# Kernel tuning notes

Measured on AMD Instinct MI355X. Metric: run time of the kernel, lower is better.

## Reference

```python
import jax, jax.numpy as jnp
import numpy as np

D_MODEL = 512
NHEAD = 8
HEAD_DIM = D_MODEL // NHEAD  # 64
ROTARY_DIM = HEAD_DIM        # rotary_dim defaults to head_dim
WINDOW = (127, 128)          # (left, right) sliding window, flash-attn convention
ROPE_BASE = 10000.0


def setup_inputs() -> dict:
    key = jax.random.key(0)
    k1, k2, k3, k4 = jax.random.split(key, 4)
    N, T = 4, 2048
    x = jax.random.normal(k1, (N, T, D_MODEL), dtype=jnp.float32)
    # Wqkv: Linear(d_model, 3*d_model, bias=False) -> weight [3*D, D]
    Wqkv_w = jax.random.normal(k2, (3 * D_MODEL, D_MODEL), dtype=jnp.float32) * (D_MODEL ** -0.5)
    # out_proj: Linear(d_model, d_model, bias=True)
    out_w = jax.random.normal(k3, (D_MODEL, D_MODEL), dtype=jnp.float32) * (D_MODEL ** -0.5)
    out_b = jax.random.normal(k4, (D_MODEL,), dtype=jnp.float32) * 0.01
    return {"x": x, "Wqkv_w": Wqkv_w, "out_w": out_w, "out_b": out_b}


def _rope_cos_sin(T, dtype):
    # flash-attn RotaryEmbedding: inv_freq over even indices of rotary_dim
    inv_freq = 1.0 / (ROPE_BASE ** (jnp.arange(0, ROTARY_DIM, 2, dtype=jnp.float32) / ROTARY_DIM))
    t = jnp.arange(T, dtype=jnp.float32)
    freqs = jnp.outer(t, inv_freq)  # [T, ROTARY_DIM//2]
    return jnp.cos(freqs).astype(dtype), jnp.sin(freqs).astype(dtype)


def _apply_rotary(x, cos, sin):
    # non-interleaved (rotate halves); x: [N, T, H, hd], rotary over first ROTARY_DIM dims
    r, rest = x[..., :ROTARY_DIM], x[..., ROTARY_DIM:]
    half = ROTARY_DIM // 2
    x1, x2 = r[..., :half], r[..., half:]
    c = cos[None, :, None, :]  # [1, T, 1, half]
    s = sin[None, :, None, :]
    rotated = jnp.concatenate([x1 * c - x2 * s, x2 * c + x1 * s], axis=-1)
    return jnp.concatenate([rotated, rest], axis=-1) if rest.shape[-1] else rotated


def reference(x, Wqkv_w, out_w, out_b):
    N, T, D = x.shape
    qkv = jnp.einsum('ntd,ed->nte', x, Wqkv_w).reshape(N, T, 3, NHEAD, HEAD_DIM)
    q, k, v = qkv[:, :, 0], qkv[:, :, 1], qkv[:, :, 2]  # each [N, T, H, hd]
    cos, sin = _rope_cos_sin(T, x.dtype)
    q = _apply_rotary(q, cos, sin)
    k = _apply_rotary(k, cos, sin)
    scale = HEAD_DIM ** -0.5
    scores = jnp.einsum('nthd,nshd->nhts', q, k) * scale  # [N, H, T, T]
    # sliding window: query i attends key j iff i - left <= j <= i + right
    i = jnp.arange(T)[:, None]
    j = jnp.arange(T)[None, :]
    mask = (j >= i - WINDOW[0]) & (j <= i + WINDOW[1])  # [T, T]
    scores = jnp.where(mask[None, None], scores, jnp.finfo(scores.dtype).min)
    attn = jax.nn.softmax(scores, axis=-1)
    ctx = jnp.einsum('nhts,nshd->nthd', attn, v).reshape(N, T, D)
    return jnp.einsum('ntd,ed->nte', ctx, out_w) + out_b
```

## Files before the change

### kernel.cpp

```cpp
#include <hip/hip_runtime.h>
#include <math.h>

#define TSEQ 2048
#define NB 4
#define DM 512
#define NH 8
#define HD 64

typedef _Float16 half8 __attribute__((ext_vector_type(8)));
typedef _Float16 half4 __attribute__((ext_vector_type(4)));
typedef float floatx4 __attribute__((ext_vector_type(4)));

#if __has_builtin(__builtin_amdgcn_exp2f)
#define EXP2F(x) __builtin_amdgcn_exp2f(x)
#else
#define EXP2F(x) exp2f(x)
#endif

__device__ __forceinline__ void gl2lds16(const _Float16* g, _Float16* l) {
  const __attribute__((address_space(1))) unsigned int* gp =
      (const __attribute__((address_space(1))) unsigned int*)(uintptr_t)g;
  __attribute__((address_space(3))) unsigned int* lp =
      (__attribute__((address_space(3))) unsigned int*)(uintptr_t)l;
  __builtin_amdgcn_global_load_lds(gp, lp, 16, 0, 0);
}


__device__ __forceinline__ void cvt8(const float* __restrict__ src, char* __restrict__ dst,
                                     int unit_src, int unit_dst) {
  const float4 a = ((const float4*)src)[2 * unit_src];
  const float4 b = ((const float4*)src)[2 * unit_src + 1];
  half8 h;
  h[0] = (_Float16)a.x; h[1] = (_Float16)a.y; h[2] = (_Float16)a.z; h[3] = (_Float16)a.w;
  h[4] = (_Float16)b.x; h[5] = (_Float16)b.y; h[6] = (_Float16)b.z; h[7] = (_Float16)b.w;
  *(half8*)(dst + (size_t)unit_dst * 16) = h;
}

__global__ void prep(const float* __restrict__ x, const float* __restrict__ wqkv,
                     const float* __restrict__ ow, char* __restrict__ ws) {
  const int i = blockIdx.x * 256 + threadIdx.x;
  if (i < 524288) {
    cvt8(x, ws, i, i);
  } else if (i < 622592) {
    const int o = i - 524288;
    cvt8(wqkv, ws + 8650752, o, o);
  } else if (i < 655360) {
    const int o = i - 622592;
    cvt8(ow, ws + 10485760, o, o);
  } else {
    const int u = i - 655360;
    float4 o4;
    {
      const int id = 2 * u, t = id >> 5, fi = id & 31;
      const float invf = powf(10000.0f, -(float)(2 * fi) * (1.0f / 64.0f));
      float s, c; sincosf((float)t * invf, &s, &c);
      o4.x = c; o4.y = s;
    }
    {
      const int id = 2 * u + 1, t = id >> 5, fi = id & 31;
      const float invf = powf(10000.0f, -(float)(2 * fi) * (1.0f / 64.0f));
      float s, c; sincosf((float)t * invf, &s, &c);
      o4.z = c; o4.w = s;
    }
    ((float4*)(ws + 46137344))[u] = o4;
  }
}

__global__ __launch_bounds__(256) void qkv_gemm_mfma(
    const _Float16* __restrict__ A, const _Float16* __restrict__ B,
    const float2* __restrict__ rope,
    _Float16* __restrict__ qb, _Float16* __restrict__ kb, _Float16* __restrict__ vT)
{
  __shared__ __align__(16) _Float16 As[128 * 32];
  __shared__ __align__(16) _Float16 Bs[128 * 32];
  const int tid = threadIdx.x;
  const int wv = tid >> 6, lane = tid & 63, quad = lane >> 4, col = lane & 15;
  const int wm = wv >> 1, we = wv & 1;
  const int m0 = blockIdx.x << 7, c0 = blockIdx.y << 7;
  const int r0 = tid >> 2, p0 = tid & 3;
  const int cA0 = (p0 - (r0 >> 1)) & 3;
  const int r1 = (tid + 256) >> 2, p1 = tid & 3;
  const int cA1 = (p1 - (r1 >> 1)) & 3;
  const _Float16* ga0 = &A[(size_t)(m0 + r0) * DM + cA0 * 8];
  const _Float16* ga1 = &A[(size_t)(m0 + r1) * DM + cA1 * 8];
  const _Float16* gb0 = &B[(size_t)(c0 + r0) * DM + cA0 * 8];
  const _Float16* gb1 = &B[(size_t)(c0 + r1) * DM + cA1 * 8];
  _Float16* la0 = &As[tid * 8];
  _Float16* la1 = &As[(tid + 256) * 8];
  _Float16* lb0 = &Bs[tid * 8];
  _Float16* lb1 = &Bs[(tid + 256) * 8];
  floatx4 acc[4][4] = {};
  for (int k0 = 0; k0 < DM; k0 += 32) {
    __syncthreads();
    gl2lds16(ga0 + k0, la0);
    gl2lds16(ga1 + k0, la1);
    gl2lds16(gb0 + k0, lb0);
    gl2lds16(gb1 + k0, lb1);
    __syncthreads();
    half8 af[4], bf[4];
#pragma unroll
    for (int mt = 0; mt < 4; mt++) {
      const int R = wm * 64 + mt * 16 + col;
      af[mt] = *(const half8*)&As[R * 32 + (((quad + (R >> 1)) & 3) << 3)];
    }
#pragma unroll
    for (int et = 0; et < 4; et++) {
      const int R = we * 64 + et * 16 + col;
      bf[et] = *(const half8*)&Bs[R * 32 + (((quad + (R >> 1)) & 3) << 3)];
    }
#pragma unroll
    for (int mt = 0; mt < 4; mt++)
#pragma unroll
      for (int et = 0; et < 4; et++)
        acc[mt][et] = __builtin_amdgcn_mfma_f32_16x16x32_f16(af[mt], bf[et], acc[mt][et], 0, 0, 0);
  }
  const int eidx = (c0 >> 6) + we;
  const int three = eidx >> 3, h = eidx & 7;
  const int mbase = m0 + wm * 64 + quad * 4;
  if (three == 2) {
#pragma unroll
    for (int mt = 0; mt < 4; mt++) {
      const int m = mbase + mt * 16;
      const int n = m >> 11, t = m & 2047;
#pragma unroll
      for (int et = 0; et < 4; et++) {
        const int dh = et * 16 + col;
        half4 hv;
#pragma unroll
        for (int r = 0; r < 4; r++) hv[r] = (_Float16)acc[mt][et][r];
        *(half4*)&vT[(size_t)(n * NH + h) * HD * TSEQ + (size_t)dh * TSEQ + t] = hv;
      }
    }
  } else {
    _Float16* dst = three ? kb : qb;
    const float scl = three ? 1.0f : 0.125f * 1.4426950408889634f;
#pragma unroll
    for (int mt = 0; mt < 4; mt++)
#pragma unroll
      for (int r = 0; r < 4; r++) {
        const int m = mbase + mt * 16 + r;
        const int n = m >> 11, t = m & 2047;
#pragma unroll
        for (int et = 0; et < 4; et++) {
          const int i = ((et & 1) << 4) + col;
          const float2 cs = rope[t * 32 + i];
          const float v = acc[mt][et][r];
          const float v2 = acc[mt][et ^ 2][r];
          const float o = (et < 2) ? (v * cs.x - v2 * cs.y) : (v * cs.x + v2 * cs.y);
          dst[((size_t)(n * NH + h) * TSEQ + t) * HD + et * 16 + col] = (_Float16)(o * scl);
        }
      }
  }
}

__global__ __launch_bounds__(256, 4) void attn_win_mfma(
    const _Float16* __restrict__ qb, const _Float16* __restrict__ kb,
    const _Float16* __restrict__ vT, _Float16* __restrict__ ctx)
{
  __shared__ __align__(16) char smem[36864];
  _Float16* Ks = (_Float16*)smem;
  _Float16* Vt = (_Float16*)(smem + 9216);
  _Float16* Ps = (_Float16*)(smem + 18432);
  _Float16* Osh = (_Float16*)(smem + 27648);

  const int tid = threadIdx.x;
  const int wv = tid >> 6;
  const int lane = tid & 63;
  const int quad = lane >> 4;
  const int col = lane & 15;
  const int nh = blockIdx.y;
  const int q0 = blockIdx.x << 6;
  const _Float16* qp = qb + (size_t)nh * TSEQ * HD;
  const _Float16* kp = kb + (size_t)nh * TSEQ * HD;
  const _Float16* vp = vT + (size_t)nh * HD * TSEQ;

  const int i_row = (wv << 4) + col;
  const int ig = q0 + i_row;
  const half8 qf0 = *(const half8*)&qp[(size_t)ig * HD + (quad << 3)];
  const half8 qf1 = *(const half8*)&qp[(size_t)ig * HD + 32 + (quad << 3)];

  float l_i = 0.0f;
  floatx4 accO[4] = {};

  const int kt0 = max(0, q0 - 127) >> 6;
  const int kt1 = min(TSEQ - 1, q0 + 191) >> 6;
  const int kr = tid >> 2, kc = (tid & 3) << 4;
  const int vd = tid >> 2, vc = (tid & 3) << 4;
  const _Float16* kpr = kp + (size_t)kr * HD + kc;
  const _Float16* vpr = vp + (size_t)vd * TSEQ + vc;

  half8 ck0 = *(const half8*)(kpr + (size_t)(kt0 << 6) * HD);
  half8 ck1 = *(const half8*)(kpr + (size_t)(kt0 << 6) * HD + 8);
  half8 cv0 = *(const half8*)(vpr + (kt0 << 6));
  half8 cv1 = *(const half8*)(vpr + (kt0 << 6) + 8);

  for (int kt = kt0; kt <= kt1; kt++) {
    const int j0 = kt << 6;
    __syncthreads();
    *(half8*)&Ks[kr * 72 + kc] = ck0;
    *(half8*)&Ks[kr * 72 + kc + 8] = ck1;
    *(half8*)&Vt[vd * 72 + vc] = cv0;
    *(half8*)&Vt[vd * 72 + vc + 8] = cv1;
    __syncthreads();

    {
      const int jn = (kt < kt1) ? (j0 + 64) : j0;
      ck0 = *(const half8*)(kpr + (size_t)jn * HD);
      ck1 = *(const half8*)(kpr + (size_t)jn * HD + 8);
      cv0 = *(const half8*)(vpr + jn);
      cv1 = *(const half8*)(vpr + jn + 8);
    }

    floatx4 S[4];
#pragma unroll
    for (int js = 0; js < 4; js++) {
      const half8 a0 = *(const half8*)&Ks[((js << 4) + col) * 72 + (quad << 3)];
      const half8 a1 = *(const half8*)&Ks[((js << 4) + col) * 72 + 32 + (quad << 3)];
      floatx4 c = {0.f, 0.f, 0.f, 0.f};
      c = __builtin_amdgcn_mfma_f32_16x16x32_f16(a0, qf0, c, 0, 0, 0);
      c = __builtin_amdgcn_mfma_f32_16x16x32_f16(a1, qf1, c, 0, 0, 0);
      S[js] = c;
    }
    const int relb = j0 - ig + 127 + (quad << 2);
#pragma unroll
    for (int js = 0; js < 4; js++) {
      half4 ph;
#pragma unroll
      for (int r = 0; r < 4; r++) {
        const bool valid = (unsigned)(relb + (js << 4) + r) < 256u;
        const float p = valid ? EXP2F(S[js][r]) : 0.0f;
        l_i += p;
        ph[r] = (_Float16)p;
      }
      *(half4*)&Ps[i_row * 72 + (js << 4) + (quad << 2)] = ph;
    }
    const half8 pa0 = *(const half8*)&Ps[i_row * 72 + (quad << 3)];
    const half8 pa1 = *(const half8*)&Ps[i_row * 72 + 32 + (quad << 3)];
#pragma unroll
    for (int d4 = 0; d4 < 4; d4++) {
      const half8 vb0 = *(const half8*)&Vt[((d4 << 4) + col) * 72 + (quad << 3)];
      const half8 vb1 = *(const half8*)&Vt[((d4 << 4) + col) * 72 + 32 + (quad << 3)];
      accO[d4] = __builtin_amdgcn_mfma_f32_16x16x32_f16(pa0, vb0, accO[d4], 0, 0, 0);
      accO[d4] = __builtin_amdgcn_mfma_f32_16x16x32_f16(pa1, vb1, accO[d4], 0, 0, 0);
    }
  }
  l_i += __shfl_xor(l_i, 16, 64);
  l_i += __shfl_xor(l_i, 32, 64);
  {
    const float linv = 1.0f / l_i;
    float l4[4];
#pragma unroll
    for (int r = 0; r < 4; r++) l4[r] = __shfl(linv, (quad << 2) + r, 64);
#pragma unroll
    for (int d4 = 0; d4 < 4; d4++)
#pragma unroll
      for (int r = 0; r < 4; r++)
        Osh[((wv << 4) + (quad << 2) + r) * 72 + (d4 << 4) + col] = (_Float16)(accO[d4][r] * l4[r]);
  }
  __syncthreads();
  {
    const int n = nh >> 3, h = nh & 7;
    const int oi = tid >> 2, oc = (tid & 3) << 4;
    _Float16* dst = &ctx[((size_t)n * TSEQ + q0 + oi) * DM + h * HD + oc];
    *(half8*)&dst[0] = *(const half8*)&Osh[oi * 72 + oc];
    *(half8*)&dst[8] = *(const half8*)&Osh[oi * 72 + oc + 8];
  }
}

__global__ __launch_bounds__(256) void out_gemm_mfma(
    const _Float16* __restrict__ A, const _Float16* __restrict__ B,
    const float* __restrict__ bias, float* __restrict__ out)
{
  __shared__ _Float16 As[128 * 40];
  __shared__ _Float16 Bs[64 * 40];
  const int tid = threadIdx.x;
  const int wv = tid >> 6, lane = tid & 63, quad = lane >> 4, col = lane & 15;
  const int wm = wv >> 1, we = wv & 1;
  const int m0 = blockIdx.x << 7, c0 = blockIdx.y << 6;
  const int sr = tid >> 1, sc = (tid & 1) << 4;
  const int br = tid >> 2, bc = (tid & 3) << 3;
  const _Float16* ap = &A[(size_t)(m0 + sr) * DM + sc];
  const _Float16* bp = &B[(size_t)(c0 + br) * DM + bc];
  floatx4 acc[4][2] = {};
  for (int k0 = 0; k0 < DM; k0 += 32) {
    const half8 a0 = *(const half8*)(ap + k0);
    const half8 a1 = *(const half8*)(ap + k0 + 8);
    const half8 b0 = *(const half8*)(bp + k0);
    __syncthreads();
    *(half8*)&As[sr * 40 + sc] = a0;
    *(half8*)&As[sr * 40 + sc + 8] = a1;
    *(half8*)&Bs[br * 40 + bc] = b0;
    __syncthreads();
    half8 af[4], bf[2];
#pragma unroll
    for (int mt = 0; mt < 4; mt++)
      af[mt] = *(const half8*)&As[(wm * 64 + mt * 16 + col) * 40 + quad * 8];
#pragma unroll
    for (int et = 0; et < 2; et++)
      bf[et] = *(const half8*)&Bs[(we * 32 + et * 16 + col) * 40 + quad * 8];
#pragma unroll
    for (int mt = 0; mt < 4; mt++)
#pragma unroll
      for (int et = 0; et < 2; et++)
        acc[mt][et] = __builtin_amdgcn_mfma_f32_16x16x32_f16(af[mt], bf[et], acc[mt][et], 0, 0, 0);
  }
  float bb[2];
#pragma unroll
  for (int et = 0; et < 2; et++) bb[et] = bias[c0 + we * 32 + et * 16 + col];
  const int mbase = m0 + wm * 64 + quad * 4;
#pragma unroll
  for (int mt = 0; mt < 4; mt++)
#pragma unroll
    for (int r = 0; r < 4; r++) {
      const int m = mbase + mt * 16 + r;
#pragma unroll
      for (int et = 0; et < 2; et++)
        out[(size_t)m * DM + c0 + we * 32 + et * 16 + col] = acc[mt][et][r] + bb[et];
    }
}

extern "C" void kernel_launch(void* const* d_in, const int* in_sizes, int n_in,
                              void* d_out, int out_size, void* d_ws, size_t ws_size,
                              hipStream_t stream) {
  const float* x    = (const float*)d_in[0];
  const float* wqkv = (const float*)d_in[1];
  const float* ow   = (const float*)d_in[2];
  const float* ob   = (const float*)d_in[3];
  char* ws = (char*)d_ws;
  _Float16* xh    = (_Float16*)(ws);
  _Float16* wqkvh = (_Float16*)(ws + 8650752);
  _Float16* owh   = (_Float16*)(ws + 10485760);
  _Float16* qbuf  = (_Float16*)(ws + 11534336);
  _Float16* kbuf  = (_Float16*)(ws + 20971520);
  _Float16* vTb   = (_Float16*)(ws + 29360128);
  _Float16* ctxh  = (_Float16*)(ws + 37748736);
  float2*   rope  = (float2*)  (ws + 46137344);

  prep<<<2688, 256, 0, stream>>>(x, wqkv, ow, ws);
  qkv_gemm_mfma<<<dim3(64, 12), 256, 0, stream>>>(xh, wqkvh, rope, qbuf, kbuf, vTb);
  attn_win_mfma<<<dim3(32, 32), 256, 0, stream>>>(qbuf, kbuf, vTb, ctxh);
  out_gemm_mfma<<<dim3(64, 8), 256, 0, stream>>>(ctxh, owh, ob, (float*)d_out);
}
```

Baseline: 130.4 us.

## Double-buffer QKV GEMM LDS tiles and prefetch out-proj GEMM operands

The QKV projection GEMM now uses two LDS buffers, so the async global-to-LDS load of the next K slice is issued before the MFMA work on the current slice. The output projection GEMM loads the next K slice's operands into registers before computing on the current tile. Both changes aim to hide global memory latency behind matrix compute, at the cost of twice the LDS in the QKV kernel (which may lower occupancy) and extra registers in the out-proj kernel. The GEMMs are only part of the total time, which also includes the attention kernel.

```diff
diff --git a/kernel.cpp b/kernel.cpp
--- a/kernel.cpp
+++ b/kernel.cpp
@@ -71,8 +71,10 @@
     const float2* __restrict__ rope,
     _Float16* __restrict__ qb, _Float16* __restrict__ kb, _Float16* __restrict__ vT)
 {
-  __shared__ __align__(16) _Float16 As[128 * 32];
-  __shared__ __align__(16) _Float16 Bs[128 * 32];
+  __shared__ __align__(16) _Float16 As0[128 * 32];
+  __shared__ __align__(16) _Float16 Bs0[128 * 32];
+  __shared__ __align__(16) _Float16 As1[128 * 32];
+  __shared__ __align__(16) _Float16 Bs1[128 * 32];
   const int tid = threadIdx.x;
   const int wv = tid >> 6, lane = tid & 63, quad = lane >> 4, col = lane & 15;
   const int wm = wv >> 1, we = wv & 1;
@@ -85,35 +87,45 @@
   const _Float16* ga1 = &A[(size_t)(m0 + r1) * DM + cA1 * 8];
   const _Float16* gb0 = &B[(size_t)(c0 + r0) * DM + cA0 * 8];
   const _Float16* gb1 = &B[(size_t)(c0 + r1) * DM + cA1 * 8];
-  _Float16* la0 = &As[tid * 8];
-  _Float16* la1 = &As[(tid + 256) * 8];
-  _Float16* lb0 = &Bs[tid * 8];
-  _Float16* lb1 = &Bs[(tid + 256) * 8];
   floatx4 acc[4][4] = {};
-  for (int k0 = 0; k0 < DM; k0 += 32) {
-    __syncthreads();
-    gl2lds16(ga0 + k0, la0);
-    gl2lds16(ga1 + k0, la1);
-    gl2lds16(gb0 + k0, lb0);
-    gl2lds16(gb1 + k0, lb1);
-    __syncthreads();
-    half8 af[4], bf[4];
-#pragma unroll
-    for (int mt = 0; mt < 4; mt++) {
-      const int R = wm * 64 + mt * 16 + col;
-      af[mt] = *(const half8*)&As[R * 32 + (((quad + (R >> 1)) & 3) << 3)];
-    }
-#pragma unroll
-    for (int et = 0; et < 4; et++) {
-      const int R = we * 64 + et * 16 + col;
-      bf[et] = *(const half8*)&Bs[R * 32 + (((quad + (R >> 1)) & 3) << 3)];
-    }
-#pragma unroll
-    for (int mt = 0; mt < 4; mt++)
-#pragma unroll
-      for (int et = 0; et < 4; et++)
-        acc[mt][et] = __builtin_amdgcn_mfma_f32_16x16x32_f16(af[mt], bf[et], acc[mt][et], 0, 0, 0);
-  }
+
+#define QKV_STAGE(AS, BS, K)                      \
+  do {                                            \
+    gl2lds16(ga0 + (K), &AS[tid * 8]);            \
+    gl2lds16(ga1 + (K), &AS[(tid + 256) * 8]);    \
+    gl2lds16(gb0 + (K), &BS[tid * 8]);            \
+    gl2lds16(gb1 + (K), &BS[(tid + 256) * 8]);    \
+  } while (0)
+
+#define QKV_COMPUTE(AS, BS)                                                   \
+  do {                                                                        \
+    half8 af[4], bf[4];                                                       \
+    _Pragma("unroll") for (int mt = 0; mt < 4; mt++) {                        \
+      const int R = wm * 64 + mt * 16 + col;                                  \
+      af[mt] = *(const half8*)&AS[R * 32 + (((quad + (R >> 1)) & 3) << 3)];   \
+    }                                                                         \
+    _Pragma("unroll") for (int et = 0; et < 4; et++) {                        \
+      const int R = we * 64 + et * 16 + col;                                  \
+      bf[et] = *(const half8*)&BS[R * 32 + (((quad + (R >> 1)) & 3) << 3)];   \
+    }                                                                         \
+    _Pragma("unroll") for (int mt = 0; mt < 4; mt++)                          \
+      _Pragma("unroll") for (int et = 0; et < 4; et++)                        \
+        acc[mt][et] =                                                         \
+            __builtin_amdgcn_mfma_f32_16x16x32_f16(af[mt], bf[et], acc[mt][et], 0, 0, 0); \
+  } while (0)
+
+  QKV_STAGE(As0, Bs0, 0);
+  for (int k0 = 0; k0 < DM; k0 += 64) {
+    __syncthreads();
+    QKV_STAGE(As1, Bs1, k0 + 32);
+    QKV_COMPUTE(As0, Bs0);
+    __syncthreads();
+    if (k0 + 64 < DM) QKV_STAGE(As0, Bs0, k0 + 64);
+    QKV_COMPUTE(As1, Bs1);
+  }
+#undef QKV_STAGE
+#undef QKV_COMPUTE
+
   const int eidx = (c0 >> 6) + we;
   const int three = eidx >> 3, h = eidx & 7;
   const int mbase = m0 + wm * 64 + quad * 4;
@@ -282,14 +294,21 @@
   const _Float16* ap = &A[(size_t)(m0 + sr) * DM + sc];
   const _Float16* bp = &B[(size_t)(c0 + br) * DM + bc];
   floatx4 acc[4][2] = {};
+  half8 a0 = *(const half8*)(ap);
+  half8 a1 = *(const half8*)(ap + 8);
+  half8 b0 = *(const half8*)(bp);
   for (int k0 = 0; k0 < DM; k0 += 32) {
-    const half8 a0 = *(const half8*)(ap + k0);
-    const half8 a1 = *(const half8*)(ap + k0 + 8);
-    const half8 b0 = *(const half8*)(bp + k0);
     __syncthreads();
     *(half8*)&As[sr * 40 + sc] = a0;
     *(half8*)&As[sr * 40 + sc + 8] = a1;
     *(half8*)&Bs[br * 40 + bc] = b0;
+    half8 an0, an1, bn0;
+    const bool more = (k0 + 32 < DM);
+    if (more) {
+      an0 = *(const half8*)(ap + k0 + 32);
+      an1 = *(const half8*)(ap + k0 + 40);
+      bn0 = *(const half8*)(bp + k0 + 32);
+    }
     __syncthreads();
     half8 af[4], bf[2];
 #pragma unroll
@@ -303,6 +322,7 @@
 #pragma unroll
       for (int et = 0; et < 2; et++)
         acc[mt][et] = __builtin_amdgcn_mfma_f32_16x16x32_f16(af[mt], bf[et], acc[mt][et], 0, 0, 0);
+    if (more) { a0 = an0; a1 = an1; b0 = bn0; }
   }
   float bb[2];
 #pragma unroll
```

Measured after the change: 125.6 us. 3.7% less time.
